# Optimization experiments

Measured on AMD Instinct MI355X. Metric: run time of the kernel, lower is better.

## Reference

```python
import jax, jax.numpy as jnp
import numpy as np

HEADS = 8


def setup_inputs() -> dict:
    key = jax.random.key(0)
    ks = jax.random.split(key, 6)
    B, N, D = 4, 2048, 512
    return {
        "x": jax.random.normal(ks[0], (B, N, D), dtype=jnp.float32),
        "pos": jax.random.uniform(ks[1], (B, N, 3), dtype=jnp.float32),
        "qkv_w": jax.random.normal(ks[2], (3 * D, D), dtype=jnp.float32) * 0.02,
        "qkv_b": jax.random.normal(ks[3], (3 * D,), dtype=jnp.float32) * 0.02,
        "out_w": jax.random.normal(ks[4], (D, D), dtype=jnp.float32) * 0.02,
        "out_b": jax.random.normal(ks[5], (D,), dtype=jnp.float32) * 0.02,
    }


def reference(x, pos, qkv_w, qkv_b, out_w, out_b):
    B, N, D = x.shape
    H = HEADS
    Dh = D // H
    scale = D ** (-0.5)  # NOTE: original uses full dim, not head dim

    # QKV projection -> [3, B, H, N, Dh]
    qkv = (x @ qkv_w.T + qkv_b).reshape(B, N, 3, H, Dh).transpose(2, 0, 3, 1, 4)
    q, k, v = qkv[0], qkv[1], qkv[2]

    # partial 3D RoPE on first 6 head dims (3 axis pairs)
    theta = pos * jnp.pi                    # [B, N, 3]
    sin = jnp.sin(theta)[:, None]           # [B, 1, N, 3] broadcasts over heads
    cos = jnp.cos(theta)[:, None]

    def rotate(t):
        x_rot = t[..., :6]
        x1 = x_rot[..., 0::2]               # [B, H, N, 3]
        x2 = x_rot[..., 1::2]
        return jnp.concatenate(
            [x1 * cos - x2 * sin, x1 * sin + x2 * cos, t[..., 6:]], axis=-1
        )

    q = rotate(q)
    k = rotate(k)

    attn = jax.nn.softmax(jnp.einsum("bhqd,bhkd->bhqk", q, k) * scale, axis=-1)
    out = jnp.einsum("bhqk,bhkd->bhqd", attn, v)          # [B, H, N, Dh]
    out = out.transpose(0, 2, 1, 3).reshape(B, N, D)
    return out @ out_w.T + out_b
```

## Files before the change

### kernel.cpp

```cpp
#include <hip/hip_runtime.h>
#include <stdint.h>

typedef __attribute__((ext_vector_type(4))) float f32x4;
typedef __attribute__((ext_vector_type(16))) float f32x16;
typedef __attribute__((ext_vector_type(8))) short bf16x8;
typedef __attribute__((ext_vector_type(4))) unsigned short u16x4;

__device__ __forceinline__ unsigned short f2bf(float f) {
    unsigned int u = __builtin_bit_cast(unsigned int, f);
    u += 0x7fffu + ((u >> 16) & 1u);
    return (unsigned short)(u >> 16);
}
__device__ __forceinline__ float bf2f(unsigned short s) {
    unsigned int u = ((unsigned int)s) << 16;
    return __builtin_bit_cast(float, u);
}
__device__ __forceinline__ float fexp2(float x) {
#if __has_builtin(__builtin_amdgcn_exp2f)
    return __builtin_amdgcn_exp2f(x);
#else
    return exp2f(x);
#endif
}
__device__ __forceinline__ unsigned int cvt_pk_bf16(float lo, float hi) {
    unsigned int r;
    asm("v_cvt_pk_bf16_f32 %0, %1, %2" : "=v"(r) : "v"(lo), "v"(hi));
    return r;
}

__global__ void k_cvt(const float* __restrict__ in, unsigned short* __restrict__ out, int n4) {
    int i = blockIdx.x * blockDim.x + threadIdx.x;
    if (i >= n4) return;
    f32x4 v = ((const f32x4*)in)[i];
    u16x4 o;
    o.x = f2bf(v.x); o.y = f2bf(v.y); o.z = f2bf(v.z); o.w = f2bf(v.w);
    ((u16x4*)out)[i] = o;
}

template<int OUT_BF16>
__global__ __launch_bounds__(256, 2)
void k_gemm_nt(const unsigned short* __restrict__ A,
               const unsigned short* __restrict__ Bm,
               const float* __restrict__ bias,
               void* __restrict__ Cout, int M, int N, int K) {
    __shared__ unsigned short As[128 * 32];
    __shared__ unsigned short Bs[128 * 32];
    const int tid = threadIdx.x;
    const int lane = tid & 63;
    const int w = tid >> 6;
    const int wr = (w >> 1) * 64, wc = (w & 1) * 64;
    const int g = lane >> 4, fr = lane & 15;

    f32x4 acc[4][4];
#pragma unroll
    for (int i = 0; i < 4; ++i)
#pragma unroll
        for (int j = 0; j < 4; ++j) acc[i][j] = f32x4{0.f, 0.f, 0.f, 0.f};

    const int srow = tid >> 2;
    const int scol = (tid & 3) * 8;
    const unsigned short* gA0 = A + (size_t)(blockIdx.x * 128 + srow) * K + scol;
    const unsigned short* gA1 = gA0 + (size_t)64 * K;
    const unsigned short* gB0 = Bm + (size_t)(blockIdx.y * 128 + srow) * K + scol;
    const unsigned short* gB1 = gB0 + (size_t)64 * K;
    char* ldsA = (char*)As + (size_t)w * 1024;
    char* ldsB = (char*)Bs + (size_t)w * 1024;

    for (int k0 = 0; k0 < K; k0 += 32) {
        __syncthreads();
        __builtin_amdgcn_global_load_lds((const __attribute__((address_space(1))) void*)(gA0 + k0),
                                         (__attribute__((address_space(3))) void*)(ldsA), 16, 0, 0);
        __builtin_amdgcn_global_load_lds((const __attribute__((address_space(1))) void*)(gA1 + k0),
                                         (__attribute__((address_space(3))) void*)(ldsA + 4096), 16, 0, 0);
        __builtin_amdgcn_global_load_lds((const __attribute__((address_space(1))) void*)(gB0 + k0),
                                         (__attribute__((address_space(3))) void*)(ldsB), 16, 0, 0);
        __builtin_amdgcn_global_load_lds((const __attribute__((address_space(1))) void*)(gB1 + k0),
                                         (__attribute__((address_space(3))) void*)(ldsB + 4096), 16, 0, 0);
        __syncthreads();
        bf16x8 af[4], bfv[4];
#pragma unroll
        for (int mi = 0; mi < 4; ++mi)
            af[mi] = *(const bf16x8*)&As[(wr + mi * 16 + fr) * 32 + g * 8];
#pragma unroll
        for (int ni = 0; ni < 4; ++ni)
            bfv[ni] = *(const bf16x8*)&Bs[(wc + ni * 16 + fr) * 32 + g * 8];
#pragma unroll
        for (int mi = 0; mi < 4; ++mi)
#pragma unroll
            for (int ni = 0; ni < 4; ++ni)
                acc[mi][ni] = __builtin_amdgcn_mfma_f32_16x16x32_bf16(af[mi], bfv[ni], acc[mi][ni], 0, 0, 0);
    }

#pragma unroll
    for (int mi = 0; mi < 4; ++mi) {
#pragma unroll
        for (int ni = 0; ni < 4; ++ni) {
            int row = blockIdx.x * 128 + wr + mi * 16 + g * 4;
            int col = blockIdx.y * 128 + wc + ni * 16 + fr;
            float bz = bias[col];
#pragma unroll
            for (int r = 0; r < 4; ++r) {
                float v = acc[mi][ni][r] + bz;
                if (OUT_BF16) ((unsigned short*)Cout)[(size_t)(row + r) * N + col] = f2bf(v);
                else          ((float*)Cout)[(size_t)(row + r) * N + col] = v;
            }
        }
    }
}

__global__ void k_rotary(const unsigned short* __restrict__ qkv,
                         const float* __restrict__ pos,
                         unsigned short* __restrict__ Qb,
                         unsigned short* __restrict__ Kb,
                         unsigned short* __restrict__ VT) {
    const float PI = 3.14159265358979323846f;
    const float QS = 0.04419417382415922f * 1.44269504088896341f;
    int cid = blockIdx.x * 256 + threadIdx.x;
    int s = cid >> 19;
    int r = cid & 524287;
    if (s < 2) {
        int m = r >> 6, c = r & 63;
        int h = c >> 3, dc = c & 7;
        int b = m >> 11, n = m & 2047;
        bf16x8 v = *(const bf16x8*)&qkv[m * 1536 + s * 512 + c * 8];
        float f[8];
#pragma unroll
        for (int i = 0; i < 8; ++i) f[i] = bf2f((unsigned short)v[i]);
        if (dc == 0) {
            float nf[6];
#pragma unroll
            for (int j = 0; j < 3; ++j) {
                float th = pos[m * 3 + j] * PI;
                float sn = __sinf(th), cs = __cosf(th);
                float x1 = f[2 * j], x2 = f[2 * j + 1];
                nf[j] = x1 * cs - x2 * sn;
                nf[3 + j] = x1 * sn + x2 * cs;
            }
#pragma unroll
            for (int j = 0; j < 6; ++j) f[j] = nf[j];
        }
        if (s == 0) {
#pragma unroll
            for (int i = 0; i < 8; ++i) f[i] *= QS;
        }
        bf16x8 o;
#pragma unroll
        for (int i = 0; i < 8; ++i) o[i] = (short)f2bf(f[i]);
        unsigned short* dst = (s == 0) ? Qb : Kb;
        *(bf16x8*)&dst[((size_t)(b * 8 + h) * 2048 + n) * 64 + dc * 8] = o;
    } else {
        int cd = r >> 13;
        int m = r & 8191;
        int b = m >> 11, n = m & 2047;
        int h = cd >> 3, d8 = (cd & 7) * 8;
        bf16x8 v = *(const bf16x8*)&qkv[m * 1536 + 1024 + cd * 8];
        int q2 = (n >> 2) & 3;
        int np = n + (q2 == 1 ? 4 : (q2 == 2 ? -4 : 0));
        size_t base = ((size_t)(b * 8 + h) * 64 + d8) * 2048 + np;
#pragma unroll
        for (int i = 0; i < 8; ++i) VT[base + (size_t)i * 2048] = (unsigned short)v[i];
    }
}

__global__ __launch_bounds__(512, 4)
void k_attn(const unsigned short* __restrict__ Qb,
            const unsigned short* __restrict__ Kb,
            const unsigned short* __restrict__ VT,
            unsigned short* __restrict__ Ob) {
    __shared__ unsigned short smem[2][2][2][4096];
    const int tid = threadIdx.x, lane = tid & 63, w = tid >> 6;
    const int wl = w & 3, half = w >> 2;
    const int l31 = lane & 31, hi = lane >> 5;
    const int bh = blockIdx.y, b = bh >> 3, h = bh & 7;
    const int qr0 = blockIdx.x * 128 + wl * 32;
    const unsigned short* Q = Qb + (size_t)bh * 2048 * 64;
    const unsigned short* K = Kb + (size_t)bh * 2048 * 64;
    const unsigned short* V = VT + (size_t)bh * 64 * 2048;
    const int thalf = half * 16;

    const int srow8 = lane >> 3;
    const int swc = ((lane & 7) ^ srow8) << 3;
    const int sA = wl, sB = wl + 4;

    bf16x8 bq[4];
#pragma unroll
    for (int ds = 0; ds < 4; ++ds)
        bq[ds] = *(const bf16x8*)&Q[(size_t)(qr0 + l31) * 64 + ds * 16 + hi * 8];

    f32x16 oT0, oT1;
#pragma unroll
    for (int i = 0; i < 16; ++i) { oT0[i] = 0.f; oT1[i] = 0.f; }
    float lpart = 0.f;

    auto stage = [&](int bsel, int t) {
        const int kv0 = t * 64;
        const unsigned short* k0 = K + (size_t)(kv0 + sA * 8 + srow8) * 64 + swc;
        const unsigned short* k1 = K + (size_t)(kv0 + sB * 8 + srow8) * 64 + swc;
        const unsigned short* v0 = V + (size_t)(sA * 8 + srow8) * 2048 + kv0 + swc;
        const unsigned short* v1 = V + (size_t)(sB * 8 + srow8) * 2048 + kv0 + swc;
        char* dk = (char*)&smem[half][0][bsel][0];
        char* dv = (char*)&smem[half][1][bsel][0];
        __builtin_amdgcn_global_load_lds((const __attribute__((address_space(1))) void*)k0,
                                         (__attribute__((address_space(3))) void*)(dk + sA * 1024), 16, 0, 0);
        __builtin_amdgcn_global_load_lds((const __attribute__((address_space(1))) void*)k1,
                                         (__attribute__((address_space(3))) void*)(dk + sB * 1024), 16, 0, 0);
        __builtin_amdgcn_global_load_lds((const __attribute__((address_space(1))) void*)v0,
                                         (__attribute__((address_space(3))) void*)(dv + sA * 1024), 16, 0, 0);
        __builtin_amdgcn_global_load_lds((const __attribute__((address_space(1))) void*)v1,
                                         (__attribute__((address_space(3))) void*)(dv + sB * 1024), 16, 0, 0);
    };

    auto pack8 = [&](const float* p) -> bf16x8 {
        union { unsigned int u[4]; bf16x8 v; } c;
        c.u[0] = cvt_pk_bf16(p[0], p[1]);
        c.u[1] = cvt_pk_bf16(p[2], p[3]);
        c.u[2] = cvt_pk_bf16(p[4], p[5]);
        c.u[3] = cvt_pk_bf16(p[6], p[7]);
        return c.v;
    };

    auto compute = [&](int bsel) {
        const unsigned short* KsC = &smem[half][0][bsel][0];
        const unsigned short* VtC = &smem[half][1][bsel][0];
        f32x16 s0, s1;
#pragma unroll
        for (int i = 0; i < 16; ++i) { s0[i] = 0.f; s1[i] = 0.f; }
        __builtin_amdgcn_s_setprio(1);
#pragma unroll
        for (int ds = 0; ds < 4; ++ds) {
            const int c = ((((ds << 1) | hi) ^ (l31 & 7)) << 3);
            bf16x8 ka0 = *(const bf16x8*)&KsC[l31 * 64 + c];
            bf16x8 ka1 = *(const bf16x8*)&KsC[(32 + l31) * 64 + c];
            s0 = __builtin_amdgcn_mfma_f32_32x32x16_bf16(ka0, bq[ds], s0, 0, 0, 0);
            s1 = __builtin_amdgcn_mfma_f32_32x32x16_bf16(ka1, bq[ds], s1, 0, 0, 0);
        }
        __builtin_amdgcn_s_setprio(0);
        float p0[16], p1[16];
        float lsum = 0.f;
#pragma unroll
        for (int r = 0; r < 16; ++r) {
            p0[r] = fexp2(s0[r]);
            p1[r] = fexp2(s1[r]);
            lsum += p0[r] + p1[r];
        }
        lpart += lsum;
        bf16x8 pb0 = pack8(p0);
        bf16x8 pb1 = pack8(p0 + 8);
        bf16x8 pb2 = pack8(p1);
        bf16x8 pb3 = pack8(p1 + 8);
        __builtin_amdgcn_s_setprio(1);
#pragma unroll
        for (int kb = 0; kb < 4; ++kb) {
            const int c = ((((kb << 1) | hi) ^ (l31 & 7)) << 3);
            bf16x8 av0 = *(const bf16x8*)&VtC[l31 * 64 + c];
            bf16x8 av1 = *(const bf16x8*)&VtC[(32 + l31) * 64 + c];
            bf16x8 pbk = (kb == 0) ? pb0 : (kb == 1) ? pb1 : (kb == 2) ? pb2 : pb3;
            oT0 = __builtin_amdgcn_mfma_f32_32x32x16_bf16(av0, pbk, oT0, 0, 0, 0);
            oT1 = __builtin_amdgcn_mfma_f32_32x32x16_bf16(av1, pbk, oT1, 0, 0, 0);
        }
        __builtin_amdgcn_s_setprio(0);
    };

    stage(0, thalf);
    int cur = 0;
#pragma unroll 1
    for (int t = 0; t < 15; ++t) {
        __builtin_amdgcn_s_barrier();
        stage(cur ^ 1, thalf + t + 1);
        asm volatile("s_waitcnt vmcnt(4)" ::: "memory");
        __builtin_amdgcn_s_barrier();
        compute(cur);
        cur ^= 1;
    }
    asm volatile("s_waitcnt vmcnt(0)" ::: "memory");
    __builtin_amdgcn_s_barrier();
    compute(cur);

    __syncthreads();
    float* mrg = (float*)&smem[0][0][0][0];
    float* slot = mrg + (size_t)(wl * 64 + lane) * 33;
    if (half) {
#pragma unroll
        for (int i = 0; i < 16; ++i) { slot[i] = oT0[i]; slot[16 + i] = oT1[i]; }
        slot[32] = lpart;
    }
    __syncthreads();
    if (!half) {
#pragma unroll
        for (int i = 0; i < 16; ++i) { oT0[i] += slot[i]; oT1[i] += slot[16 + i]; }
        float lf = lpart + slot[32];
        lf += __shfl_xor(lf, 32, 64);
        float il = 1.f / lf;
        size_t rowbase = (size_t)(b * 2048 + qr0 + l31) * 512 + h * 64;
#pragma unroll
        for (int grp = 0; grp < 4; ++grp) {
            u16x4 o0, o1;
#pragma unroll
            for (int i = 0; i < 4; ++i) {
                o0[i] = f2bf(oT0[grp * 4 + i] * il);
                o1[i] = f2bf(oT1[grp * 4 + i] * il);
            }
            int dv0 = grp * 8 + 4 * hi;
            *(u16x4*)&Ob[rowbase + dv0] = o0;
            *(u16x4*)&Ob[rowbase + 32 + dv0] = o1;
        }
    }
}

extern "C" void kernel_launch(void* const* d_in, const int* in_sizes, int n_in,
                              void* d_out, int out_size, void* d_ws, size_t ws_size,
                              hipStream_t stream) {
    const float* x     = (const float*)d_in[0];
    const float* pos   = (const float*)d_in[1];
    const float* qkv_w = (const float*)d_in[2];
    const float* qkv_b = (const float*)d_in[3];
    const float* out_w = (const float*)d_in[4];
    const float* out_b = (const float*)d_in[5];
    float* out = (float*)d_out;

    unsigned short* Xb   = (unsigned short*)d_ws;
    unsigned short* W1b  = Xb   + (size_t)8192 * 512;
    unsigned short* W2b  = W1b  + (size_t)1536 * 512;
    unsigned short* QKVb = W2b  + (size_t)512 * 512;
    unsigned short* Qb   = QKVb + (size_t)8192 * 1536;
    unsigned short* Kb   = Qb   + (size_t)4194304;
    unsigned short* VTb  = Kb   + (size_t)4194304;
    unsigned short* Ob   = VTb  + (size_t)4194304;

    k_cvt<<<4096, 256, 0, stream>>>(x, Xb, 8192 * 512 / 4);
    k_cvt<<<768, 256, 0, stream>>>(qkv_w, W1b, 1536 * 512 / 4);
    k_cvt<<<256, 256, 0, stream>>>(out_w, W2b, 512 * 512 / 4);
    k_gemm_nt<1><<<dim3(64, 12), 256, 0, stream>>>(Xb, W1b, qkv_b, QKVb, 8192, 1536, 512);
    k_rotary<<<6144, 256, 0, stream>>>(QKVb, pos, Qb, Kb, VTb);
    k_attn<<<dim3(16, 32), 512, 0, stream>>>(Qb, Kb, VTb, Ob);
    k_gemm_nt<0><<<dim3(64, 4), 256, 0, stream>>>(Ob, W2b, out_b, out, 8192, 512, 512);
}
```

Baseline: 101.8 us.

## Merge conversion kernels, deepen GEMM K-tile with swizzled LDS, remap attention grid

The three fp32-to-bf16 conversion launches become a single kernel that writes the contiguous workspace (Xb, W1b, W2b are laid out back to back). The GEMM K-tile grows from 32 to 64, with an XOR-swizzled LDS layout to avoid bank conflicts, so each tile feeds twice as many MFMAs per barrier pair. The attention grid becomes 1D, with block IDs remapped so that consecutive blocks are spread across heads, which may help XCD/L2 locality. The trade-off is more LDS per GEMM block (32 KB), which may affect occupancy.

```diff
diff --git a/kernel.cpp b/kernel.cpp
--- a/kernel.cpp
+++ b/kernel.cpp
@@ -28,10 +28,17 @@
     return r;
 }
 
-__global__ void k_cvt(const float* __restrict__ in, unsigned short* __restrict__ out, int n4) {
+__global__ void k_cvt3(const float* __restrict__ x,
+                       const float* __restrict__ w1,
+                       const float* __restrict__ w2,
+                       unsigned short* __restrict__ out) {
+    const int C1 = 1048576;
+    const int C2 = 196608;
     int i = blockIdx.x * blockDim.x + threadIdx.x;
-    if (i >= n4) return;
-    f32x4 v = ((const f32x4*)in)[i];
+    f32x4 v;
+    if (i < C1)            v = ((const f32x4*)x)[i];
+    else if (i < C1 + C2)  v = ((const f32x4*)w1)[i - C1];
+    else                   v = ((const f32x4*)w2)[i - C1 - C2];
     u16x4 o;
     o.x = f2bf(v.x); o.y = f2bf(v.y); o.z = f2bf(v.z); o.w = f2bf(v.w);
     ((u16x4*)out)[i] = o;
@@ -43,8 +50,8 @@
                const unsigned short* __restrict__ Bm,
                const float* __restrict__ bias,
                void* __restrict__ Cout, int M, int N, int K) {
-    __shared__ unsigned short As[128 * 32];
-    __shared__ unsigned short Bs[128 * 32];
+    __shared__ unsigned short As[128 * 64];
+    __shared__ unsigned short Bs[128 * 64];
     const int tid = threadIdx.x;
     const int lane = tid & 63;
     const int w = tid >> 6;
@@ -57,38 +64,42 @@
 #pragma unroll
         for (int j = 0; j < 4; ++j) acc[i][j] = f32x4{0.f, 0.f, 0.f, 0.f};
 
-    const int srow = tid >> 2;
-    const int scol = (tid & 3) * 8;
-    const unsigned short* gA0 = A + (size_t)(blockIdx.x * 128 + srow) * K + scol;
-    const unsigned short* gA1 = gA0 + (size_t)64 * K;
-    const unsigned short* gB0 = Bm + (size_t)(blockIdx.y * 128 + srow) * K + scol;
-    const unsigned short* gB1 = gB0 + (size_t)64 * K;
-    char* ldsA = (char*)As + (size_t)w * 1024;
-    char* ldsB = (char*)Bs + (size_t)w * 1024;
-
-    for (int k0 = 0; k0 < K; k0 += 32) {
+    const int srow8 = lane >> 3;
+    const int swc = ((lane & 7) ^ srow8) * 8;
+    const unsigned short* Abase = A + (size_t)(blockIdx.x * 128 + w * 8 + srow8) * K + swc;
+    const unsigned short* Bbase = Bm + (size_t)(blockIdx.y * 128 + w * 8 + srow8) * K + swc;
+    char* ldsA = (char*)As + w * 1024;
+    char* ldsB = (char*)Bs + w * 1024;
+
+    for (int k0 = 0; k0 < K; k0 += 64) {
         __syncthreads();
-        __builtin_amdgcn_global_load_lds((const __attribute__((address_space(1))) void*)(gA0 + k0),
-                                         (__attribute__((address_space(3))) void*)(ldsA), 16, 0, 0);
-        __builtin_amdgcn_global_load_lds((const __attribute__((address_space(1))) void*)(gA1 + k0),
-                                         (__attribute__((address_space(3))) void*)(ldsA + 4096), 16, 0, 0);
-        __builtin_amdgcn_global_load_lds((const __attribute__((address_space(1))) void*)(gB0 + k0),
-                                         (__attribute__((address_space(3))) void*)(ldsB), 16, 0, 0);
-        __builtin_amdgcn_global_load_lds((const __attribute__((address_space(1))) void*)(gB1 + k0),
-                                         (__attribute__((address_space(3))) void*)(ldsB + 4096), 16, 0, 0);
+#pragma unroll
+        for (int i = 0; i < 4; ++i) {
+            __builtin_amdgcn_global_load_lds(
+                (const __attribute__((address_space(1))) void*)(Abase + (size_t)i * 32 * K + k0),
+                (__attribute__((address_space(3))) void*)(ldsA + i * 4096), 16, 0, 0);
+            __builtin_amdgcn_global_load_lds(
+                (const __attribute__((address_space(1))) void*)(Bbase + (size_t)i * 32 * K + k0),
+                (__attribute__((address_space(3))) void*)(ldsB + i * 4096), 16, 0, 0);
+        }
         __syncthreads();
-        bf16x8 af[4], bfv[4];
-#pragma unroll
-        for (int mi = 0; mi < 4; ++mi)
-            af[mi] = *(const bf16x8*)&As[(wr + mi * 16 + fr) * 32 + g * 8];
-#pragma unroll
-        for (int ni = 0; ni < 4; ++ni)
-            bfv[ni] = *(const bf16x8*)&Bs[(wc + ni * 16 + fr) * 32 + g * 8];
-#pragma unroll
-        for (int mi = 0; mi < 4; ++mi)
+        bf16x8 af[2][4], bfv[2][4];
+#pragma unroll
+        for (int kk = 0; kk < 2; ++kk) {
+#pragma unroll
+            for (int mi = 0; mi < 4; ++mi)
+                af[kk][mi] = *(const bf16x8*)&As[(wr + mi * 16 + fr) * 64 + (((kk * 4 + g) ^ (fr & 7)) * 8)];
 #pragma unroll
             for (int ni = 0; ni < 4; ++ni)
-                acc[mi][ni] = __builtin_amdgcn_mfma_f32_16x16x32_bf16(af[mi], bfv[ni], acc[mi][ni], 0, 0, 0);
+                bfv[kk][ni] = *(const bf16x8*)&Bs[(wc + ni * 16 + fr) * 64 + (((kk * 4 + g) ^ (fr & 7)) * 8)];
+        }
+#pragma unroll
+        for (int kk = 0; kk < 2; ++kk)
+#pragma unroll
+            for (int mi = 0; mi < 4; ++mi)
+#pragma unroll
+                for (int ni = 0; ni < 4; ++ni)
+                    acc[mi][ni] = __builtin_amdgcn_mfma_f32_16x16x32_bf16(af[kk][mi], bfv[kk][ni], acc[mi][ni], 0, 0, 0);
     }
 
 #pragma unroll
@@ -171,8 +182,11 @@
     const int tid = threadIdx.x, lane = tid & 63, w = tid >> 6;
     const int wl = w & 3, half = w >> 2;
     const int l31 = lane & 31, hi = lane >> 5;
-    const int bh = blockIdx.y, b = bh >> 3, h = bh & 7;
-    const int qr0 = blockIdx.x * 128 + wl * 32;
+    const int bid = blockIdx.x;
+    const int bh = (bid & 7) * 4 + ((bid >> 3) >> 4);
+    const int qb = (bid >> 3) & 15;
+    const int b = bh >> 3, h = bh & 7;
+    const int qr0 = qb * 128 + wl * 32;
     const unsigned short* Q = Qb + (size_t)bh * 2048 * 64;
     const unsigned short* K = Kb + (size_t)bh * 2048 * 64;
     const unsigned short* V = VT + (size_t)bh * 64 * 2048;
@@ -327,11 +341,9 @@
     unsigned short* VTb  = Kb   + (size_t)4194304;
     unsigned short* Ob   = VTb  + (size_t)4194304;
 
-    k_cvt<<<4096, 256, 0, stream>>>(x, Xb, 8192 * 512 / 4);
-    k_cvt<<<768, 256, 0, stream>>>(qkv_w, W1b, 1536 * 512 / 4);
-    k_cvt<<<256, 256, 0, stream>>>(out_w, W2b, 512 * 512 / 4);
+    k_cvt3<<<5120, 256, 0, stream>>>(x, qkv_w, out_w, Xb);
     k_gemm_nt<1><<<dim3(64, 12), 256, 0, stream>>>(Xb, W1b, qkv_b, QKVb, 8192, 1536, 512);
     k_rotary<<<6144, 256, 0, stream>>>(QKVb, pos, Qb, Kb, VTb);
-    k_attn<<<dim3(16, 32), 512, 0, stream>>>(Qb, Kb, VTb, Ob);
+    k_attn<<<512, 512, 0, stream>>>(Qb, Kb, VTb, Ob);
     k_gemm_nt<0><<<dim3(64, 4), 256, 0, stream>>>(Ob, W2b, out_b, out, 8192, 512, 512);
 }
```

After: 91.84 us. 1.11x faster.
